# Performance work log

Measured on AMD Instinct MI355X. Metric: run time of the kernel, lower is better.

The kernel has to match this reference:

```python
import jax, jax.numpy as jnp
import numpy as np

EPS = 1e-8
LOG_EPS = 1e-20  # guard before log for categorical logits


def setup_inputs() -> dict:
    key = jax.random.key(0)
    B, T, K, I = 64, 1024, 512, 4
    k1, k2, k3, k4 = jax.random.split(key, 4)
    data = jax.random.randint(k1, (B, T), 0, K)
    masks = jax.random.bernoulli(k2, 0.5, (B, T)).astype(jnp.float32)
    init_p = jax.random.uniform(k3, (K,), dtype=jnp.float32)
    init_p = init_p / (init_p.sum() + EPS)
    P = jax.random.uniform(k4, (K, K), dtype=jnp.float32)
    P = P / (P.sum(axis=1, keepdims=True) + EPS)
    return {
        "data": data,
        "masks": masks,
        "init_probability": init_p,
        "transition_probability": P,
        "nb_imputation": I,
    }


def _forward_filter(data, masks, init_p, P):
    """HMM forward filtering. Returns messages [T, B, K]."""
    B, T = data.shape
    K = init_p.shape[0]
    oh = jax.nn.one_hot(data, K, dtype=init_p.dtype)      # [B,T,K]
    m = masks[..., None]                                   # [B,T,1]
    msg0 = init_p[None, :] * (1.0 - m[:, 0]) + m[:, 0] * oh[:, 0]
    msg0 = msg0 / (msg0.sum(-1, keepdims=True) + EPS)

    def step(prev, xs):
        oh_i, m_i = xs                                     # [B,K],[B,1]
        msg = (prev @ P) * (1.0 - m_i) + m_i * oh_i
        msg = msg / msg.sum(-1, keepdims=True)             # source uses no eps for t>=1
        return msg, msg

    xs = (jnp.moveaxis(oh[:, 1:], 1, 0), jnp.moveaxis(m[:, 1:], 1, 0))
    _, rest = jax.lax.scan(step, msg0, xs)                 # [T-1,B,K]
    return jnp.concatenate([msg0[None], rest], axis=0)    # [T,B,K]


def reference(data, masks, init_probability, transition_probability, nb_imputation):
    B, T = data.shape
    K = init_probability.shape[0]
    I = nb_imputation
    P = transition_probability

    messages = _forward_filter(data, masks, init_probability, P)  # [T,B,K]

    key = jax.random.key(42)
    k_last, k_seq = jax.random.split(key)

    # --- sample last timestep ---
    logp_last = jnp.log(messages[-1] + LOG_EPS)            # [B,K]
    s_last = jax.random.categorical(k_last, logp_last[:, None, :], shape=(B, I))
    m_last = masks[:, -1][:, None] > 0
    d_last = data[:, -1][:, None]
    # NOTE: faithful to source, last step uses mask*sample + (1-mask)*data
    out_last = jnp.where(m_last, s_last, d_last)           # [B,I]

    # --- backward sampling scan, t = T-2 .. 0 ---
    PT = P.T                                               # row j = P[:, j]
    keys = jax.random.split(k_seq, T - 1)

    def bstep(s_next, xs):
        msg_i, m_i, d_i, k_i = xs                          # [B,K],[B],[B],key
        trans = PT[s_next]                                 # [B,I,K] = P[:, s_next].T
        w = msg_i[:, None, :] * (trans + 1.0 / K)
        w = w / (w.sum(-1, keepdims=True) + EPS)
        s = jax.random.categorical(k_i, jnp.log(w + LOG_EPS))  # [B,I]
        # other steps: (1-mask)*sample + mask*data
        s = jnp.where(m_i[:, None] > 0, d_i[:, None], s)
        return s, s

    xs = (
        messages[: T - 1][::-1],                           # [T-1,B,K]
        masks[:, : T - 1].T[::-1],                         # [T-1,B]
        data[:, : T - 1].T[::-1],                          # [T-1,B]
        keys,
    )
    _, samples = jax.lax.scan(bstep, out_last, xs)         # [T-1,B,I] reversed time
    samples = samples[::-1]
    out = jnp.concatenate([samples, out_last[None]], axis=0)  # [T,B,I]
    return jnp.moveaxis(out, 0, 2)                         # [B,I,T]
```

## Files before the change

kernel.cpp:

```cpp
#include <hip/hip_runtime.h>
#include <stdint.h>


#define JAX_PARTITIONABLE 1

#define B_ 64
#define T_ 1024
#define K_ 512
#define I_ 4
#define NCHAIN (B_ * I_)
#define POWSLOT (513 * 512)
#define LMAX_WANT 8
#define MAXRUNS 32769
#define BWD_BLOCKS 8192

typedef double f64x4 __attribute__((ext_vector_type(4)));

__host__ __device__ inline void tf2x32(uint32_t k0, uint32_t k1, uint32_t c0, uint32_t c1,
                                       uint32_t& o0, uint32_t& o1) {
  uint32_t ks2 = k0 ^ k1 ^ 0x1BD11BDAu;
  uint32_t x0 = c0 + k0;
  uint32_t x1 = c1 + k1;
#define TFR(r) { x0 += x1; x1 = (x1 << (r)) | (x1 >> (32 - (r))); x1 ^= x0; }
  TFR(13) TFR(15) TFR(26) TFR(6)
  x0 += k1; x1 += ks2 + 1u;
  TFR(17) TFR(29) TFR(16) TFR(24)
  x0 += ks2; x1 += k0 + 2u;
  TFR(13) TFR(15) TFR(26) TFR(6)
  x0 += k0; x1 += k1 + 3u;
  TFR(17) TFR(29) TFR(16) TFR(24)
  x0 += k1; x1 += ks2 + 4u;
  TFR(13) TFR(15) TFR(26) TFR(6)
  x0 += ks2; x1 += k0 + 5u;
#undef TFR
  o0 = x0; o1 = x1;
}

__device__ inline uint32_t rng_bits(uint32_t kj0, uint32_t kj1, uint32_t e) {
#if JAX_PARTITIONABLE
  uint32_t a, b;
  tf2x32(kj0, kj1, 0u, e, a, b);
  return a ^ b;
#else
  const uint32_t HALF = (uint32_t)(NCHAIN * K_ / 2);
  uint32_t a, b;
  if (e < HALF) { tf2x32(kj0, kj1, e, e + HALF, a, b); return a; }
  else          { tf2x32(kj0, kj1, e - HALF, e, a, b); return b; }
#endif
}

__device__ inline float gumbel_scale(uint32_t bits) {
  float f = __uint_as_float((bits >> 9) | 0x3F800000u) - 1.0f;
  float u = f + 1.17549435e-38f;
  int iu = __float_as_int(u);
  float ef = (float)((iu >> 23) - 127);
  float m = __int_as_float((iu & 0x007fffff) | 0x3f800000);
  int big = m > 1.41421356f;
  m = big ? m * 0.5f : m;
  ef = big ? ef + 1.0f : ef;
  float fm = m - 1.0f;
  float r = fm * __builtin_amdgcn_rcpf(m + 1.0f);
  float r2 = r * r;
  float p = fmaf(r2, fmaf(r2, fmaf(r2, fmaf(r2, 0.11111111f, 0.14285715f),
                                   0.2f), 0.33333334f), 1.0f);
  float logu = fmaf(ef, 0.69314718f, (r + r) * p);
  return -__builtin_amdgcn_rcpf(logu);
}

__device__ inline void step_key(uint32_t ks0, uint32_t ks1, int j, uint32_t& kj0, uint32_t& kj1) {
#if JAX_PARTITIONABLE
  tf2x32(ks0, ks1, 0u, (uint32_t)j, kj0, kj1);
#else
  const int N = T_ - 1;
  uint32_t o0, o1;
  int v = 2 * j;
  if (v < N) { tf2x32(ks0, ks1, (uint32_t)v, (uint32_t)(v + N), o0, o1); kj0 = o0; }
  else       { tf2x32(ks0, ks1, (uint32_t)(v - N), (uint32_t)v, o0, o1); kj0 = o1; }
  v = 2 * j + 1;
  if (v < N) { tf2x32(ks0, ks1, (uint32_t)v, (uint32_t)(v + N), o0, o1); kj1 = o0; }
  else       { tf2x32(ks0, ks1, (uint32_t)(v - N), (uint32_t)v, o0, o1); kj1 = o1; }
#endif
}

__global__ __launch_bounds__(256) void setup_fused(
    const float* __restrict__ P, const float* __restrict__ initp,
    float* __restrict__ POW0, float* __restrict__ PTp,
    float* __restrict__ INITROW, float* __restrict__ V1,
    int* __restrict__ runCount, int* __restrict__ maxLdev,
    uint32_t* __restrict__ KEY0, uint32_t* __restrict__ KEY1,
    uint32_t ks0, uint32_t ks1) {
  int blk = blockIdx.x;
  if (blk < 1024) {
    int id = blk * 256 + threadIdx.x;
    int r = id >> 9, c = id & 511;
    float v = P[id];
    POW0[id] = v;
    PTp[c * 512 + r] = v + 0.001953125f;
    if (id < 512) INITROW[id] = initp[id];
    if (id == 0) { *runCount = 0; *maxLdev = 1; }
  } else if (blk < 1536) {
    int c = blk - 1024;
    int t = threadIdx.x;
    double acc = (double)initp[t] * (double)P[t * 512 + c]
               + (double)initp[t + 256] * (double)P[(t + 256) * 512 + c];
#pragma unroll
    for (int o = 32; o >= 1; o >>= 1) acc += __shfl_down(acc, o);
    __shared__ double sred[4];
    if ((t & 63) == 0) sred[t >> 6] = acc;
    __syncthreads();
    if (t == 0) V1[c] = (float)((sred[0] + sred[1]) + (sred[2] + sred[3]));
  } else {
    int j = (blk - 1536) * 256 + threadIdx.x;
    if (j < T_ - 1) {
      uint32_t a, b;
      step_key(ks0, ks1, j, a, b);
      KEY0[j] = a; KEY1[j] = b;
    }
  }
}

__global__ __launch_bounds__(1024) void setup_offsets_par(
    const int* __restrict__ data, const float* __restrict__ masks,
    int* __restrict__ off, int lmax, int initoff,
    int* __restrict__ runs, int* __restrict__ runCount, int* __restrict__ maxLdev) {
  __shared__ int prevObs[1024];
  __shared__ int nextObs[1024];
  int b = blockIdx.x;
  int t = threadIdx.x;
  bool obs = masks[b * T_ + t] > 0.0f;
  prevObs[t] = obs ? t : -1;
  nextObs[t] = obs ? t : T_;
  __syncthreads();
  for (int o = 1; o < 1024; o <<= 1) {
    int pv = (t >= o) ? prevObs[t - o] : -1;
    int nv = (t + o < 1024) ? nextObs[t + o] : T_;
    __syncthreads();
    if (pv > prevObs[t]) prevObs[t] = pv;
    if (nv < nextObs[t]) nextObs[t] = nv;
    __syncthreads();
  }
  int t0 = (t > 0) ? prevObs[t - 1] : -1;
  int idx = b * T_ + t;
  if (obs) off[idx] = -1;
  else if (t0 >= 0) {
    int L = t - t0; if (L > lmax) L = lmax;
    off[idx] = (L - 1) * POWSLOT + data[b * T_ + t0] * 512;
  } else if (t == 0) off[idx] = initoff;
  else {
    int L = t; if (L > lmax) L = lmax;
    off[idx] = (L - 1) * POWSLOT + 512 * 512;
  }
  if (!obs && t <= T_ - 2 && (t == 0 || masks[b * T_ + t - 1] > 0.0f)) {
    int te = nextObs[t] - 1; if (te > T_ - 2) te = T_ - 2;
    int r = atomicAdd(runCount, 1);
    if (r < MAXRUNS) {
      runs[r] = (b << 20) | (t << 10) | te;
      int maxL = (t == 0) ? te : (te - t + 1);
      if (maxL > 1) atomicMax(maxLdev, maxL);
    }
  }
}

__global__ __launch_bounds__(256) void power_gemm_mfma(float* __restrict__ POW, int m,
                                                       int lmax, const int* __restrict__ maxLdev) {
  int y = blockIdx.y;
  {
    int gate = *maxLdev; if (gate > lmax) gate = lmax;
    if (y + 1 + m > gate) return;
  }
  const float* A  = POW + (size_t)y * POWSLOT;
  const float* Bm = POW + (size_t)(m - 1) * POWSLOT;
  float* C        = POW + (size_t)(y + m) * POWSLOT;
  __shared__ double As[32][33];
  __shared__ double Bs[32][33];
  int tid = threadIdx.x;
  int lane = tid & 63;
  int wv = tid >> 6;
  int wr = wv >> 1, wc = wv & 1;
  int q = lane >> 4, r16 = lane & 15;
  int r0 = (blockIdx.x >> 4) * 32;
  int c0 = (blockIdx.x & 15) * 32;

  f64x4 z = {0.0, 0.0, 0.0, 0.0};
  f64x4 d1 = __builtin_amdgcn_mfma_f64_16x16x4f64((double)r16, 1.0, z, 0, 0, 0);
  f64x4 d2 = __builtin_amdgcn_mfma_f64_16x16x4f64(1.0, (double)r16, z, 0, 0, 0);
  int ir[4], ic[4];
#pragma unroll
  for (int v = 0; v < 4; ++v) {
    ir[v] = (((int)d1[v]) >> 2) & 15;
    ic[v] = (((int)d2[v]) >> 2) & 15;
  }

  int sr = tid >> 3;
  int sk4 = (tid & 7) * 4;
  int ar = r0 + sr; if (ar > 512) ar = 512;

  f64x4 acc = {0.0, 0.0, 0.0, 0.0};
  for (int kc = 0; kc < 512; kc += 32) {
    float4 av = *(const float4*)(A + (size_t)ar * 512 + kc + sk4);
    float4 bv = *(const float4*)(Bm + (size_t)(kc + sr) * 512 + c0 + sk4);
    __syncthreads();
    As[sk4 + 0][sr] = (double)av.x;
    As[sk4 + 1][sr] = (double)av.y;
    As[sk4 + 2][sr] = (double)av.z;
    As[sk4 + 3][sr] = (double)av.w;
    Bs[sr][sk4 + 0] = (double)bv.x;
    Bs[sr][sk4 + 1] = (double)bv.y;
    Bs[sr][sk4 + 2] = (double)bv.z;
    Bs[sr][sk4 + 3] = (double)bv.w;
    __syncthreads();
#pragma unroll
    for (int ks = 0; ks < 8; ++ks) {
      double a = As[ks * 4 + q][wr * 16 + r16];
      double b = Bs[ks * 4 + q][wc * 16 + r16];
      acc = __builtin_amdgcn_mfma_f64_16x16x4f64(a, b, acc, 0, 0, 0);
    }
  }
#pragma unroll
  for (int v = 0; v < 4; ++v) {
    int gr = r0 + wr * 16 + ir[v];
    int gc = c0 + wc * 16 + ic[v];
    if (gr < 513) C[(size_t)gr * 512 + gc] = (float)acc[v];
  }
}

__global__ __launch_bounds__(256) void backward_run(
    const int* __restrict__ data, const float* __restrict__ masks,
    const float* __restrict__ wsF, const int* __restrict__ off,
    const float* __restrict__ PTp,
    const uint32_t* __restrict__ KEY0, const uint32_t* __restrict__ KEY1,
    const int* __restrict__ runs, const int* __restrict__ runCount,
    int* __restrict__ out) {
  {
    int id = blockIdx.x * 256 + threadIdx.x;
    if (id < NCHAIN * T_) {
      int t = id & (T_ - 1);
      int b = id >> 12;
      if (t == T_ - 1 || masks[b * T_ + t] > 0.0f) out[id] = data[b * T_ + t];
    }
  }
  int lane = threadIdx.x & 63;
  int wv = threadIdx.x >> 6;
  int wid = blockIdx.x * 4 + wv;
  const int NW = BWD_BLOCKS * 4;
  int total = *runCount;
  if (total > MAXRUNS) total = MAXRUNS;
  total <<= 2;
  const float* wsL = wsF + (lane << 3);
  const float* ptL = PTp + (lane << 3);
  for (int u = wid; u < total; u += NW) {
    int run = runs[u >> 2];
    int ci = u & 3;
    int b = run >> 20, ta = (run >> 10) & 1023, tb = run & 1023;
    int s = data[b * T_ + tb + 1];
    uint32_t ebase = ((uint32_t)b << 11) | ((uint32_t)ci << 9) | ((uint32_t)(lane << 3));
    const int* offb = off + b * T_;
    int* outp = out + (((b << 2) | ci) * T_);
    for (int t = tb; t >= ta; --t) {
      int j = (T_ - 2) - t;
      uint32_t kj0 = KEY0[j], kj1 = KEY1[j];
      int o = offb[t];
      float4 m0 = *(const float4*)(wsL + o);
      float4 m1 = *(const float4*)(wsL + o + 4);
      const float* prow = ptL + ((size_t)s << 9);
      float4 p0 = *(const float4*)(prow);
      float4 p1 = *(const float4*)(prow + 4);
      float x0 = fmaf(m0.x, p0.x, 1e-20f) * gumbel_scale(rng_bits(kj0, kj1, ebase + 0u));
      float x1 = fmaf(m0.y, p0.y, 1e-20f) * gumbel_scale(rng_bits(kj0, kj1, ebase + 1u));
      float x2 = fmaf(m0.z, p0.z, 1e-20f) * gumbel_scale(rng_bits(kj0, kj1, ebase + 2u));
      float x3 = fmaf(m0.w, p0.w, 1e-20f) * gumbel_scale(rng_bits(kj0, kj1, ebase + 3u));
      float x4 = fmaf(m1.x, p1.x, 1e-20f) * gumbel_scale(rng_bits(kj0, kj1, ebase + 4u));
      float x5 = fmaf(m1.y, p1.y, 1e-20f) * gumbel_scale(rng_bits(kj0, kj1, ebase + 5u));
      float x6 = fmaf(m1.z, p1.z, 1e-20f) * gumbel_scale(rng_bits(kj0, kj1, ebase + 6u));
      float x7 = fmaf(m1.w, p1.w, 1e-20f) * gumbel_scale(rng_bits(kj0, kj1, ebase + 7u));
      float bv = x0; int bj = 0;
      if (x1 > bv) { bv = x1; bj = 1; }
      if (x2 > bv) { bv = x2; bj = 2; }
      if (x3 > bv) { bv = x3; bj = 3; }
      if (x4 > bv) { bv = x4; bj = 4; }
      if (x5 > bv) { bv = x5; bj = 5; }
      if (x6 > bv) { bv = x6; bj = 6; }
      if (x7 > bv) { bv = x7; bj = 7; }
      float wm = bv;
#pragma unroll
      for (int d = 1; d < 64; d <<= 1) wm = fmaxf(wm, __shfl_xor(wm, d));
      unsigned long long bal = __ballot(bv == wm);
      int wl = __ffsll(bal) - 1;
      int jw = __shfl(bj, wl);
      s = (wl << 3) + jw;
      if (lane == 0) outp[t] = s;
    }
  }
}

extern "C" void kernel_launch(void* const* d_in, const int* in_sizes, int n_in,
                              void* d_out, int out_size, void* d_ws, size_t ws_size,
                              hipStream_t stream) {
  const int* data = (const int*)d_in[0];
  const float* masks = (const float*)d_in[1];
  const float* initp = (const float*)d_in[2];
  const float* P = (const float*)d_in[3];
  int* out = (int*)d_out;

  int lmax = LMAX_WANT;
  {
    long long fixed = 512LL * 512 + 512 + (long long)B_ * T_ + 2 * (T_ - 1) + MAXRUNS + 64;
    long long avail = (long long)(ws_size / 4) - fixed;
    long long fit = avail / POWSLOT;
    if (fit < lmax) lmax = (fit < 1) ? 1 : (int)fit;
  }
  float* wsF = (float*)d_ws;
  float* POW = wsF;
  float* PTp = wsF + (size_t)lmax * POWSLOT;
  float* INITROW = PTp + 512 * 512;
  int* off = (int*)(INITROW + 512);
  uint32_t* KEY0 = (uint32_t*)(off + B_ * T_);
  uint32_t* KEY1 = KEY0 + (T_ - 1);
  int* runs = (int*)(KEY1 + (T_ - 1));
  int* runCount = runs + MAXRUNS;
  int* maxLdev = runCount + 1;
  int initoff = lmax * POWSLOT + 512 * 512;

  uint32_t ks0, ks1;
#if JAX_PARTITIONABLE
  tf2x32(0u, 42u, 0u, 1u, ks0, ks1);
#else
  {
    uint32_t a0, b0, a1, b1;
    tf2x32(0u, 42u, 0u, 2u, a0, b0);
    tf2x32(0u, 42u, 1u, 3u, a1, b1);
    ks0 = b0; ks1 = b1;
  }
#endif

  hipLaunchKernelGGL(setup_fused, dim3(1540), dim3(256), 0, stream,
                     P, initp, POW, PTp, INITROW, POW + 512 * 512,
                     runCount, maxLdev, KEY0, KEY1, ks0, ks1);
  hipLaunchKernelGGL(setup_offsets_par, dim3(B_), dim3(1024), 0, stream,
                     data, masks, off, lmax, initoff, runs, runCount, maxLdev);
  int m = 1;
  while (m < lmax) {
    int count = lmax - m; if (count > m) count = m;
    hipLaunchKernelGGL(power_gemm_mfma, dim3(17 * 16, count), dim3(256), 0, stream,
                       POW, m, lmax, maxLdev);
    m += count;
  }
  hipLaunchKernelGGL(backward_run, dim3(BWD_BLOCKS), dim3(256), 0, stream,
                     data, masks, wsF, off, PTp, KEY0, KEY1, runs, runCount, out);
}
```

Before: 319.1 us.

## Sort backward-sampling runs by length to balance work across blocks

```diff
diff --git a/kernel.cpp b/kernel.cpp
--- a/kernel.cpp
+++ b/kernel.cpp
@@ -13,6 +13,8 @@
 #define LMAX_WANT 8
 #define MAXRUNS 32769
 #define BWD_BLOCKS 8192
+#define GEMM_BLOCKS (17 * 16)
+#define SORT_BLOCKS 129
 
 typedef double f64x4 __attribute__((ext_vector_type(4)));
 
@@ -86,7 +88,7 @@
     const float* __restrict__ P, const float* __restrict__ initp,
     float* __restrict__ POW0, float* __restrict__ PTp,
     float* __restrict__ INITROW, float* __restrict__ V1,
-    int* __restrict__ runCount, int* __restrict__ maxLdev,
+    int* __restrict__ runCount, int* __restrict__ maxLdev, int* __restrict__ histcur,
     uint32_t* __restrict__ KEY0, uint32_t* __restrict__ KEY1,
     uint32_t ks0, uint32_t ks1) {
   int blk = blockIdx.x;
@@ -97,20 +99,15 @@
     POW0[id] = v;
     PTp[c * 512 + r] = v + 0.001953125f;
     if (id < 512) INITROW[id] = initp[id];
+    if (id < 128) histcur[id] = 0;
     if (id == 0) { *runCount = 0; *maxLdev = 1; }
-  } else if (blk < 1536) {
-    int c = blk - 1024;
-    int t = threadIdx.x;
-    double acc = (double)initp[t] * (double)P[t * 512 + c]
-               + (double)initp[t + 256] * (double)P[(t + 256) * 512 + c];
-#pragma unroll
-    for (int o = 32; o >= 1; o >>= 1) acc += __shfl_down(acc, o);
-    __shared__ double sred[4];
-    if ((t & 63) == 0) sred[t >> 6] = acc;
-    __syncthreads();
-    if (t == 0) V1[c] = (float)((sred[0] + sred[1]) + (sred[2] + sred[3]));
+  } else if (blk < 1026) {
+    int c = (blk - 1024) * 256 + threadIdx.x;
+    double acc = 0.0;
+    for (int j = 0; j < 512; ++j) acc += (double)initp[j] * (double)P[j * 512 + c];
+    V1[c] = (float)acc;
   } else {
-    int j = (blk - 1536) * 256 + threadIdx.x;
+    int j = (blk - 1026) * 256 + threadIdx.x;
     if (j < T_ - 1) {
       uint32_t a, b;
       step_key(ks0, ks1, j, a, b);
@@ -122,7 +119,8 @@
 __global__ __launch_bounds__(1024) void setup_offsets_par(
     const int* __restrict__ data, const float* __restrict__ masks,
     int* __restrict__ off, int lmax, int initoff,
-    int* __restrict__ runs, int* __restrict__ runCount, int* __restrict__ maxLdev) {
+    int* __restrict__ runs, int* __restrict__ runCount, int* __restrict__ maxLdev,
+    int* __restrict__ hist) {
   __shared__ int prevObs[1024];
   __shared__ int nextObs[1024];
   int b = blockIdx.x;
@@ -155,14 +153,37 @@
     int r = atomicAdd(runCount, 1);
     if (r < MAXRUNS) {
       runs[r] = (b << 20) | (t << 10) | te;
+      int steps = te - t + 1;
+      int bkt = steps < 63 ? steps : 63;
+      atomicAdd(&hist[bkt], 1);
       int maxL = (t == 0) ? te : (te - t + 1);
       if (maxL > 1) atomicMax(maxLdev, maxL);
     }
   }
 }
 
-__global__ __launch_bounds__(256) void power_gemm_mfma(float* __restrict__ POW, int m,
-                                                       int lmax, const int* __restrict__ maxLdev) {
+__global__ __launch_bounds__(256) void power_gemm_mfma(
+    float* __restrict__ POW, int m, int lmax, const int* __restrict__ maxLdev,
+    int sortN, const int* __restrict__ runs, const int* __restrict__ runCount,
+    const int* __restrict__ hist, int* __restrict__ cursor,
+    int* __restrict__ runsSorted) {
+  if (blockIdx.x >= GEMM_BLOCKS) {
+    if (sortN && blockIdx.y == 0) {
+      int i = (blockIdx.x - GEMM_BLOCKS) * 256 + threadIdx.x;
+      int total = *runCount; if (total > MAXRUNS) total = MAXRUNS;
+      if (i < total) {
+        int r = runs[i];
+        int ta = (r >> 10) & 1023, tb = r & 1023;
+        int steps = tb - ta + 1;
+        int bkt = steps < 63 ? steps : 63;
+        int base = 0;
+        for (int l = bkt + 1; l < 64; ++l) base += hist[l];
+        int slot = base + atomicAdd(&cursor[bkt], 1);
+        runsSorted[slot] = r;
+      }
+    }
+    return;
+  }
   int y = blockIdx.y;
   {
     int gate = *maxLdev; if (gate > lmax) gate = lmax;
@@ -304,7 +325,8 @@
 
   int lmax = LMAX_WANT;
   {
-    long long fixed = 512LL * 512 + 512 + (long long)B_ * T_ + 2 * (T_ - 1) + MAXRUNS + 64;
+    long long fixed = 512LL * 512 + 512 + (long long)B_ * T_ + 2 * (T_ - 1)
+                      + 2LL * MAXRUNS + 256;
     long long avail = (long long)(ws_size / 4) - fixed;
     long long fit = avail / POWSLOT;
     if (fit < lmax) lmax = (fit < 1) ? 1 : (int)fit;
@@ -319,6 +341,10 @@
   int* runs = (int*)(KEY1 + (T_ - 1));
   int* runCount = runs + MAXRUNS;
   int* maxLdev = runCount + 1;
+  int* histcur = runCount + 2;
+  int* hist = histcur;
+  int* cursor = histcur + 64;
+  int* runsSorted = histcur + 128;
   int initoff = lmax * POWSLOT + 512 * 512;
 
   uint32_t ks0, ks1;
@@ -333,18 +359,27 @@
   }
 #endif
 
-  hipLaunchKernelGGL(setup_fused, dim3(1540), dim3(256), 0, stream,
+  hipLaunchKernelGGL(setup_fused, dim3(1030), dim3(256), 0, stream,
                      P, initp, POW, PTp, INITROW, POW + 512 * 512,
-                     runCount, maxLdev, KEY0, KEY1, ks0, ks1);
+                     runCount, maxLdev, histcur, KEY0, KEY1, ks0, ks1);
   hipLaunchKernelGGL(setup_offsets_par, dim3(B_), dim3(1024), 0, stream,
-                     data, masks, off, lmax, initoff, runs, runCount, maxLdev);
-  int m = 1;
+                     data, masks, off, lmax, initoff, runs, runCount, maxLdev, hist);
+  int m = 1, first = 1;
   while (m < lmax) {
     int count = lmax - m; if (count > m) count = m;
-    hipLaunchKernelGGL(power_gemm_mfma, dim3(17 * 16, count), dim3(256), 0, stream,
-                       POW, m, lmax, maxLdev);
+    hipLaunchKernelGGL(power_gemm_mfma,
+                       dim3(GEMM_BLOCKS + (first ? SORT_BLOCKS : 0), count), dim3(256), 0, stream,
+                       POW, m, lmax, maxLdev,
+                       first, runs, runCount, hist, cursor, runsSorted);
+    first = 0;
     m += count;
   }
+  if (first) {
+    hipLaunchKernelGGL(power_gemm_mfma,
+                       dim3(GEMM_BLOCKS + SORT_BLOCKS, 1), dim3(256), 0, stream,
+                       POW, 1, lmax, maxLdev,
+                       1, runs, runCount, hist, cursor, runsSorted);
+  }
   hipLaunchKernelGGL(backward_run, dim3(BWD_BLOCKS), dim3(256), 0, stream,
-                     data, masks, wsF, off, PTp, KEY0, KEY1, runs, runCount, out);
-}
+                     data, masks, wsF, off, PTp, KEY0, KEY1, runsSorted, runCount, out);
+}
```

New measurement: 548.3 us. +71.8%, slower.
